# Optimization experiments

Measured on AMD Instinct MI355X. Metric: run time of the kernel, lower is better.

## Reference

```python
import jax, jax.numpy as jnp
import numpy as np

N, E = 50000, 800000
IN_DIM, EDGE_DIM, HID, OUT_DIM, L = 128, 16, 64, 8, 4
MSG_EPS = 1e-7  # GENConv eps added to relu(msg)


def layer_norm(x, g, b, eps=1e-5):
    mu = x.mean(-1, keepdims=True)
    var = ((x - mu) ** 2).mean(-1, keepdims=True)
    return (x - mu) * jax.lax.rsqrt(var + eps) * g + b


def segment_softmax(logits, seg, num_segments):
    # numerically stable softmax over edges grouped by destination node
    m = jax.ops.segment_max(logits, seg, num_segments=num_segments)
    m = jnp.where(jnp.isfinite(m), m, 0.0)
    e = jnp.exp(logits - m[seg])
    s = jax.ops.segment_sum(e, seg, num_segments=num_segments)
    return e / (s[seg] + 1e-16)


def gen_conv(x, src, dst, ea, t, W1, b1, g1, be1, W2, b2):
    # GENConv: message = relu(x_j + e_ij) + eps, softmax-aggregate by dst, add root, MLP [h->2h->h]
    msg = jax.nn.relu(x[src] + ea) + MSG_EPS          # [E, H]
    alpha = segment_softmax(msg * t, dst, x.shape[0]) # [E, H]
    agg = jax.ops.segment_sum(msg * alpha, dst, num_segments=x.shape[0])  # [N, H]
    h = agg + x
    h = jax.nn.relu(layer_norm(h @ W1 + b1, g1, be1))  # [N, 2H]
    return h @ W2 + b2                                 # [N, H]


def setup_inputs() -> dict:
    key = jax.random.key(0)
    ks = jax.random.split(key, 16)
    sc = 0.05
    inp = {
        "x": jax.random.normal(ks[0], (N, IN_DIM), jnp.float32),
        "edge_attr": jax.random.normal(ks[1], (E, EDGE_DIM), jnp.float32),
        "node_W": jax.random.normal(ks[2], (IN_DIM, HID), jnp.float32) * sc,
        "node_b": jnp.zeros((HID,), jnp.float32),
        "edge_W": jax.random.normal(ks[3], (EDGE_DIM, HID), jnp.float32) * sc,
        "edge_b": jnp.zeros((HID,), jnp.float32),
        "conv_t": jnp.ones((L,), jnp.float32),
        "conv_W1": jax.random.normal(ks[4], (L, HID, 2 * HID), jnp.float32) * sc,
        "conv_b1": jnp.zeros((L, 2 * HID), jnp.float32),
        "conv_g1": jnp.ones((L, 2 * HID), jnp.float32),
        "conv_be1": jnp.zeros((L, 2 * HID), jnp.float32),
        "conv_W2": jax.random.normal(ks[5], (L, 2 * HID, HID), jnp.float32) * sc,
        "conv_b2": jnp.zeros((L, HID), jnp.float32),
        "ln_g": jnp.ones((L, HID), jnp.float32),
        "ln_b": jnp.zeros((L, HID), jnp.float32),
        "lin_W": jax.random.normal(ks[6], (HID, OUT_DIM), jnp.float32) * sc,
        "lin_b": jnp.zeros((OUT_DIM,), jnp.float32),
        "edge_index": jax.random.randint(ks[7], (2, E), 0, N, jnp.int64),
    }
    return inp


def reference(x, edge_attr, node_W, node_b, edge_W, edge_b,
              conv_t, conv_W1, conv_b1, conv_g1, conv_be1, conv_W2, conv_b2,
              ln_g, ln_b, lin_W, lin_b, edge_index):
    src, dst = edge_index[0], edge_index[1]  # flow: source_to_target
    h = x @ node_W + node_b
    ea = edge_attr @ edge_W + edge_b
    # first layer: conv only (DeeperGCN applies layers[0].conv directly)
    h = gen_conv(h, src, dst, ea, conv_t[0], conv_W1[0], conv_b1[0],
                 conv_g1[0], conv_be1[0], conv_W2[0], conv_b2[0])
    # res+ blocks: x + conv(dropout(relu(norm(x)))); dropout inactive (eval)
    for i in range(1, L):
        z = jax.nn.relu(layer_norm(h, ln_g[i], ln_b[i]))
        h = h + gen_conv(z, src, dst, ea, conv_t[i], conv_W1[i], conv_b1[i],
                         conv_g1[i], conv_be1[i], conv_W2[i], conv_b2[i])
    h = jax.nn.relu(layer_norm(h, ln_g[0], ln_b[0]))
    return h @ lin_W + lin_b
```

## Files before the change

kernel.cpp:

```cpp
#include <hip/hip_runtime.h>
#include <hip/hip_fp16.h>

#define N_NODES 50000
#define N_EDGES 800000
#define IN_DIM  128
#define EDGE_DIM 16
#define HID     64
#define HID2    128
#define OUT_DIM 8
#define N_LAYERS 4
#define NBUCK   391
#define CCHUNK  4096
#define CBLOCKS 196

typedef _Float16 half8 __attribute__((ext_vector_type(8)));
typedef float floatx4 __attribute__((ext_vector_type(4)));

static __device__ __forceinline__ float bcast(float v, int l) {
    return __uint_as_float(__builtin_amdgcn_readlane(__float_as_uint(v), l));
}

__global__ __launch_bounds__(256, 4) void chist_kernel(
    const int* __restrict__ dsts, int* __restrict__ ccnt)
{
    __shared__ int lh[NBUCK];
    for (int i = threadIdx.x; i < NBUCK; i += 256) lh[i] = 0;
    __syncthreads();
    const int base = blockIdx.x * CCHUNK;
#pragma unroll
    for (int i = 0; i < 16; ++i) {
        const int e = base + i * 256 + threadIdx.x;
        if (e < N_EDGES) atomicAdd(&lh[dsts[e] >> 7], 1);
    }
    __syncthreads();
    for (int i = threadIdx.x; i < NBUCK; i += 256)
        if (lh[i]) atomicAdd(&ccnt[i], lh[i]);
}

__global__ __launch_bounds__(256, 1) void cscan_kernel(
    const int* __restrict__ ccnt, int* __restrict__ coff, int* __restrict__ ccur)
{
    __shared__ int part[512];
    const int t = threadIdx.x;
    part[t]       = (t < NBUCK)       ? ccnt[t]       : 0;
    part[t + 256] = (t + 256 < NBUCK) ? ccnt[t + 256] : 0;
    __syncthreads();
    for (int off = 1; off < 512; off <<= 1) {
        const int v0 = (t >= off) ? part[t - off] : 0;
        const int v1 = (t + 256 >= off) ? part[t + 256 - off] : 0;
        __syncthreads();
        part[t] += v0; part[t + 256] += v1;
        __syncthreads();
    }
    if (t < NBUCK) { const int ex = (t > 0) ? part[t - 1] : 0; coff[t] = ex; ccur[t] = ex; }
    const int i2 = t + 256;
    if (i2 < NBUCK) { coff[i2] = part[i2 - 1]; ccur[i2] = part[i2 - 1]; }
    if (t == 0) coff[NBUCK] = part[NBUCK - 1];
}

__global__ __launch_bounds__(256, 4) void cscatter_kernel(
    const int* __restrict__ srcs, const int* __restrict__ dsts,
    int* __restrict__ ccur, uint2* __restrict__ tmp)
{
    __shared__ int lh[NBUCK], lbase[NBUCK], lrank[NBUCK];
    for (int i = threadIdx.x; i < NBUCK; i += 256) { lh[i] = 0; lrank[i] = 0; }
    __syncthreads();
    const int base = blockIdx.x * CCHUNK;
    int myd[16], mys[16];
#pragma unroll
    for (int i = 0; i < 16; ++i) {
        const int e = base + i * 256 + threadIdx.x;
        if (e < N_EDGES) {
            myd[i] = dsts[e]; mys[i] = srcs[e];
            atomicAdd(&lh[myd[i] >> 7], 1);
        } else myd[i] = -1;
    }
    __syncthreads();
    for (int i = threadIdx.x; i < NBUCK; i += 256) {
        const int c = lh[i];
        lbase[i] = c ? atomicAdd(&ccur[i], c) : 0;
    }
    __syncthreads();
#pragma unroll
    for (int i = 0; i < 16; ++i) {
        if (myd[i] >= 0) {
            const int e = base + i * 256 + threadIdx.x;
            const int b = myd[i] >> 7;
            const int r = atomicAdd(&lrank[b], 1);
            tmp[lbase[b] + r] =
                make_uint2((unsigned)mys[i] | ((unsigned)myd[i] << 16),
                           (unsigned)e);
        }
    }
}

__global__ __launch_bounds__(256, 1) void fsort_kernel(
    const uint2* __restrict__ tmp, const int* __restrict__ coff,
    unsigned* __restrict__ sd2, int* __restrict__ eid)
{
    __shared__ uint2 ebuf[4096];
    __shared__ int lh[128], lsc[128];
    const int b = blockIdx.x;
    const int lo = coff[b];
    const int cnt = coff[b + 1] - lo;
    if (threadIdx.x < 128) lh[threadIdx.x] = 0;
    __syncthreads();
    for (int i = threadIdx.x; i < cnt; i += 256) {
        const uint2 v = tmp[lo + i];
        ebuf[i] = v;
        atomicAdd(&lh[(int)(v.x >> 16) - b * 128], 1);
    }
    __syncthreads();
    if (threadIdx.x < 128) lsc[threadIdx.x] = lh[threadIdx.x];
    __syncthreads();
    for (int off = 1; off < 128; off <<= 1) {
        int v = 0;
        if (threadIdx.x < 128 && threadIdx.x >= off) v = lsc[threadIdx.x - off];
        __syncthreads();
        if (threadIdx.x < 128) lsc[threadIdx.x] += v;
        __syncthreads();
    }
    if (threadIdx.x < 128) lh[threadIdx.x] = lsc[threadIdx.x] - lh[threadIdx.x];
    __syncthreads();
    for (int i = threadIdx.x; i < cnt; i += 256) {
        const uint2 v = ebuf[i];
        const int d = (int)(v.x >> 16) - b * 128;
        const int pos = atomicAdd(&lh[d], 1);
        sd2[lo + pos] = v.x;
        eid[lo + pos] = (int)v.y;
    }
}

__global__ __launch_bounds__(256, 2) void node_proj_kernel(
    const float* __restrict__ x, const float* __restrict__ W,
    const float* __restrict__ b, float* __restrict__ h, __half* __restrict__ zh)
{
    __shared__ float xs[4][IN_DIM];
    const int c = threadIdx.x & 63;
    const int local_n = threadIdx.x >> 6;
    float w[IN_DIM];
#pragma unroll
    for (int k = 0; k < IN_DIM; ++k) w[k] = W[k * HID + c];
    const float bias = b[c];

    for (int base = blockIdx.x * 4; base < N_NODES; base += gridDim.x * 4) {
        __syncthreads();
#pragma unroll
        for (int i = 0; i < 2; ++i) {
            int idx = threadIdx.x + i * 256;
            int nn = idx >> 7, kk = idx & 127;
            xs[nn][kk] = x[(base + nn) * IN_DIM + kk];
        }
        __syncthreads();
        const int n = base + local_n;
        float acc = bias;
#pragma unroll
        for (int k4 = 0; k4 < IN_DIM / 4; ++k4) {
            float4 xv = ((const float4*)xs[local_n])[k4];
            acc = fmaf(xv.x, w[k4 * 4 + 0], acc);
            acc = fmaf(xv.y, w[k4 * 4 + 1], acc);
            acc = fmaf(xv.z, w[k4 * 4 + 2], acc);
            acc = fmaf(xv.w, w[k4 * 4 + 3], acc);
        }
        h[n * HID + c] = acc;
        zh[n * HID + c] = __float2half(acc);
    }
}

__global__ __launch_bounds__(256, 4) void edge_emb_kernel(
    const float* __restrict__ ea, const float* __restrict__ W,
    const float* __restrict__ b, const int* __restrict__ eid,
    __half* __restrict__ eah)
{
    __shared__ __half lds_t[4][16 * HID];
    const int lane = threadIdx.x & 63;
    const int waveid = threadIdx.x >> 6;
    const int wave = (blockIdx.x * 256 + threadIdx.x) >> 6;
    const int nwaves = gridDim.x * 4;
    const int m = lane & 15, q = lane >> 4;
    const int NT = N_EDGES / 16;

    half8 bf[4];
#pragma unroll
    for (int blk = 0; blk < 4; ++blk) {
#pragma unroll
        for (int i = 0; i < 8; ++i) {
            const int k = q * 8 + i;
            bf[blk][i] = (k < EDGE_DIM)
                ? (_Float16)W[k * HID + blk * 16 + m] : (_Float16)0.f;
        }
    }
    float bv[4];
#pragma unroll
    for (int blk = 0; blk < 4; ++blk) bv[blk] = b[blk * 16 + m];

    const int ed = lane >> 3, ch = lane & 7;

    for (int tile = wave; tile < NT; tile += nwaves) {
        const int e0 = tile * 16;
        const int eidx = eid[e0 + m];
        half8 af;
#pragma unroll
        for (int i = 0; i < 8; ++i) af[i] = (_Float16)0.f;
        if (q < 2) {
            const float4* ap =
                (const float4*)(ea + (size_t)eidx * EDGE_DIM + q * 8);
            const float4 lo = ap[0];
            const float4 hi = ap[1];
            af[0] = (_Float16)lo.x; af[1] = (_Float16)lo.y;
            af[2] = (_Float16)lo.z; af[3] = (_Float16)lo.w;
            af[4] = (_Float16)hi.x; af[5] = (_Float16)hi.y;
            af[6] = (_Float16)hi.z; af[7] = (_Float16)hi.w;
        }
        floatx4 c[4];
#pragma unroll
        for (int blk = 0; blk < 4; ++blk) {
            floatx4 cin = {bv[blk], bv[blk], bv[blk], bv[blk]};
            c[blk] = __builtin_amdgcn_mfma_f32_16x16x32_f16(
                af, bf[blk], cin, 0, 0, 0);
        }
#pragma unroll
        for (int blk = 0; blk < 4; ++blk)
#pragma unroll
            for (int r = 0; r < 4; ++r)
                lds_t[waveid][(q * 4 + r) * HID + blk * 16 + m] =
                    __float2half(c[blk][r]);
        const float4 v0 =
            *(const float4*)&lds_t[waveid][ed * HID + ch * 8];
        const float4 v1 =
            *(const float4*)&lds_t[waveid][(8 + ed) * HID + ch * 8];
        ((float4*)(eah + (size_t)(e0 + ed) * HID))[ch] = v0;
        ((float4*)(eah + (size_t)(e0 + 8 + ed) * HID))[ch] = v1;
    }
}

__global__ __launch_bounds__(256, 3) void edge_agg_kernel(
    const __half* __restrict__ zh, const __half* __restrict__ eah,
    const unsigned* __restrict__ sd2,
    const float* __restrict__ conv_t, int layer,
    float* __restrict__ p, float* __restrict__ s)
{
    const int lane = threadIdx.x & 63;
    const int wave = (blockIdx.x * 256 + threadIdx.x) >> 6;
    const int nwaves = gridDim.x * 4;
    const float t2 = conv_t[layer] * 1.4426950408889634f;
    const int NT = N_EDGES / 64;

    const _Float16* zf = (const _Float16*)zh;
    const _Float16* ef = (const _Float16*)eah;

    for (int tile = wave; tile < NT; tile += nwaves) {
        const int e0 = tile * 64;
        const unsigned sdv = sd2[e0 + lane];
        const _Float16* erow = ef + (size_t)e0 * HID + lane;

        _Float16 ez[64];
#pragma unroll
        for (int k = 0; k < 64; ++k) ez[k] = erow[(size_t)k * HID];

        const int sv = (int)(sdv & 0xffffu);
        const int dv = (int)(sdv >> 16);
        const int pv = __shfl_up(dv, 1, 64);
        const unsigned long long bmask = __ballot(dv != pv) & ~1ull;

        _Float16 za[16], zb[16];
#pragma unroll
        for (int k = 0; k < 16; ++k) {
            const int a = __builtin_amdgcn_readlane(sv, k);
            za[k] = zf[(size_t)a * HID + lane];
        }

        float S = 0.f, P = 0.f;
        int cur = __builtin_amdgcn_readlane(dv, 0);
#pragma unroll
        for (int g = 0; g < 4; ++g) {
            if (g < 3) {
#pragma unroll
                for (int k = 0; k < 16; ++k) {
                    const int a = __builtin_amdgcn_readlane(sv, (g + 1) * 16 + k);
                    zb[k] = zf[(size_t)a * HID + lane];
                }
            }
#pragma unroll
            for (int k = 0; k < 16; ++k) {
                const int j = g * 16 + k;
                if (bmask & (1ull << j)) {
                    unsafeAtomicAdd(&s[(size_t)cur * HID + lane], S);
                    unsafeAtomicAdd(&p[(size_t)cur * HID + lane], P);
                    S = 0.f; P = 0.f;
                    cur = __builtin_amdgcn_readlane(dv, j);
                }
                _Float16 mh = za[k] + ez[j];
                mh = mh > (_Float16)0.f ? mh : (_Float16)0.f;
                const float mm = (float)mh + 1e-7f;
                const float xx = __builtin_amdgcn_exp2f(mm * t2);
                S += xx;
                P = fmaf(mm, xx, P);
            }
            if (g < 3) {
#pragma unroll
                for (int k = 0; k < 16; ++k) za[k] = zb[k];
            }
        }
        unsafeAtomicAdd(&s[(size_t)cur * HID + lane], S);
        unsafeAtomicAdd(&p[(size_t)cur * HID + lane], P);
    }
}

__global__ __launch_bounds__(256, 3) void node_mm1_kernel(
    float* __restrict__ p, float* __restrict__ s,
    const __half* __restrict__ zh,
    const float* __restrict__ W1, const float* __restrict__ b1,
    const float* __restrict__ g1, const float* __restrict__ be1,
    __half* __restrict__ vh)
{
    const int lane = threadIdx.x & 63;
    const int wave = (blockIdx.x * 256 + threadIdx.x) >> 6;
    const int nwaves = gridDim.x * 4;

    float wa[HID], wb[HID];
#pragma unroll
    for (int k = 0; k < HID; ++k) {
        wa[k] = W1[k * HID2 + lane];
        wb[k] = W1[k * HID2 + 64 + lane];
    }
    const float ba = b1[lane],  bb = b1[64 + lane];
    const float ga = g1[lane],  gb = g1[64 + lane];
    const float ca = be1[lane], cb = be1[64 + lane];

    for (int n = wave; n < N_NODES; n += nwaves) {
        const int idx = n * HID + lane;
        const float pv = p[idx];
        const float sv = s[idx];
        const float zv = __half2float(zh[idx]);
        p[idx] = 0.f;
        s[idx] = 0.f;
        const float hv = pv / (sv + 1e-16f) + zv;

        float a0 = 0.f, a1 = 0.f, c0 = 0.f, c1 = 0.f;
#pragma unroll
        for (int k = 0; k < 32; ++k) {
            const float x0 = bcast(hv, k);
            const float x1 = bcast(hv, k + 32);
            a0 = fmaf(x0, wa[k], a0);
            c0 = fmaf(x0, wb[k], c0);
            a1 = fmaf(x1, wa[k + 32], a1);
            c1 = fmaf(x1, wb[k + 32], c1);
        }
        const float ua = (a0 + a1) + ba;
        const float ub = (c0 + c1) + bb;

        float sum = ua + ub;
#pragma unroll
        for (int o = 1; o < 64; o <<= 1) sum += __shfl_xor(sum, o, 64);
        const float mu = sum * (1.f / 128.f);
        const float da = ua - mu, db = ub - mu;
        float q = fmaf(da, da, db * db);
#pragma unroll
        for (int o = 1; o < 64; o <<= 1) q += __shfl_xor(q, o, 64);
        const float rstd = rsqrtf(q * (1.f / 128.f) + 1e-5f);
        const float ya = da * rstd * ga + ca;
        const float yb = db * rstd * gb + cb;
        vh[(size_t)n * HID2 + lane]      = __float2half(ya > 0.f ? ya : 0.f);
        vh[(size_t)n * HID2 + 64 + lane] = __float2half(yb > 0.f ? yb : 0.f);
    }
}

__global__ __launch_bounds__(256, 3) void node_mm2_kernel(
    const __half* __restrict__ vh,
    const float* __restrict__ W2, const float* __restrict__ b2,
    const float* __restrict__ lng, const float* __restrict__ lnb,
    float* __restrict__ h, __half* __restrict__ zh, int residual)
{
    const int lane = threadIdx.x & 63;
    const int wave = (blockIdx.x * 256 + threadIdx.x) >> 6;
    const int nwaves = gridDim.x * 4;

    float wa[HID2 / 2], wb[HID2 / 2];
#pragma unroll
    for (int k = 0; k < HID2 / 2; ++k) {
        wa[k] = W2[k * HID + lane];
        wb[k] = W2[(k + 64) * HID + lane];
    }
    const float bias = b2[lane];
    const float g = lng[lane];
    const float be = lnb[lane];

    for (int n = wave; n < N_NODES; n += nwaves) {
        const float f0 = __half2float(vh[(size_t)n * HID2 + lane]);
        const float f1 = __half2float(vh[(size_t)n * HID2 + 64 + lane]);

        float a0 = 0.f, a1 = 0.f, c0 = 0.f, c1 = 0.f;
#pragma unroll
        for (int k = 0; k < 32; ++k) {
            const float x0 = bcast(f0, k);
            const float x1 = bcast(f0, k + 32);
            const float x2 = bcast(f1, k);
            const float x3 = bcast(f1, k + 32);
            a0 = fmaf(x0, wa[k], a0);
            a1 = fmaf(x1, wa[k + 32], a1);
            c0 = fmaf(x2, wb[k], c0);
            c1 = fmaf(x3, wb[k + 32], c1);
        }
        const float acc = (a0 + a1) + (c0 + c1) + bias;

        const int idx = n * HID + lane;
        const float hn = residual ? (h[idx] + acc) : acc;
        h[idx] = hn;

        float sum = hn;
#pragma unroll
        for (int o = 1; o < 64; o <<= 1) sum += __shfl_xor(sum, o, 64);
        const float mu = sum * (1.f / 64.f);
        const float d = hn - mu;
        float q = d * d;
#pragma unroll
        for (int o = 1; o < 64; o <<= 1) q += __shfl_xor(q, o, 64);
        const float var = q * (1.f / 64.f);
        const float y = d * rsqrtf(var + 1e-5f) * g + be;
        zh[idx] = __float2half(y > 0.f ? y : 0.f);
    }
}

__global__ __launch_bounds__(256, 4) void final_kernel(
    const __half* __restrict__ zh, const float* __restrict__ Wl,
    const float* __restrict__ bl, float* __restrict__ out)
{
    __shared__ float wl[HID * OUT_DIM];
    for (int i = threadIdx.x; i < HID * OUT_DIM; i += 256) wl[i] = Wl[i];
    __syncthreads();
    const int total = N_NODES * OUT_DIM;
    for (int idx = blockIdx.x * 256 + threadIdx.x; idx < total;
         idx += gridDim.x * 256) {
        const int n = idx >> 3, o = idx & 7;
        const __half2* zp = (const __half2*)(zh + (size_t)n * HID);
        float acc = bl[o];
#pragma unroll
        for (int k2 = 0; k2 < HID / 2; ++k2) {
            const float2 f = __half22float2(zp[k2]);
            acc = fmaf(f.x, wl[(k2 * 2 + 0) * OUT_DIM + o], acc);
            acc = fmaf(f.y, wl[(k2 * 2 + 1) * OUT_DIM + o], acc);
        }
        out[idx] = acc;
    }
}

extern "C" void kernel_launch(void* const* d_in, const int* in_sizes, int n_in,
                              void* d_out, int out_size, void* d_ws, size_t ws_size,
                              hipStream_t stream)
{
    const float* x         = (const float*)d_in[0];
    const float* edge_attr = (const float*)d_in[1];
    const float* node_W    = (const float*)d_in[2];
    const float* node_b    = (const float*)d_in[3];
    const float* edge_W    = (const float*)d_in[4];
    const float* edge_b    = (const float*)d_in[5];
    const float* conv_t    = (const float*)d_in[6];
    const float* conv_W1   = (const float*)d_in[7];
    const float* conv_b1   = (const float*)d_in[8];
    const float* conv_g1   = (const float*)d_in[9];
    const float* conv_be1  = (const float*)d_in[10];
    const float* conv_W2   = (const float*)d_in[11];
    const float* conv_b2   = (const float*)d_in[12];
    const float* ln_g      = (const float*)d_in[13];
    const float* ln_b      = (const float*)d_in[14];
    const float* lin_W     = (const float*)d_in[15];
    const float* lin_b     = (const float*)d_in[16];
    const int*   edge_index= (const int*)d_in[17];
    const int*   srcs = edge_index;
    const int*   dsts = edge_index + N_EDGES;
    float* out = (float*)d_out;

    float* h   = (float*)d_ws;
    float* p   = h   + N_NODES * HID;
    float* s   = p   + N_NODES * HID;
    __half* vh  = (__half*)(s + N_NODES * HID);
    __half* zh  = vh + (size_t)N_NODES * HID2;
    __half* eah = zh + (size_t)N_NODES * HID;
    uint2* tmp  = (uint2*)(eah + (size_t)N_EDGES * HID);
    unsigned* sd2 = (unsigned*)(tmp + N_EDGES);
    int* eid    = (int*)(sd2 + N_EDGES);
    int* ccnt   = eid + N_EDGES;
    int* coff   = ccnt + NBUCK;
    int* ccur   = coff + NBUCK + 1;

    hipMemsetAsync(ccnt, 0, (size_t)NBUCK * sizeof(int), stream);
    chist_kernel<<<CBLOCKS, 256, 0, stream>>>(dsts, ccnt);
    cscan_kernel<<<1, 256, 0, stream>>>(ccnt, coff, ccur);
    cscatter_kernel<<<CBLOCKS, 256, 0, stream>>>(srcs, dsts, ccur, tmp);
    fsort_kernel<<<NBUCK, 256, 0, stream>>>(tmp, coff, sd2, eid);

    node_proj_kernel<<<2048, 256, 0, stream>>>(x, node_W, node_b, h, zh);
    edge_emb_kernel<<<3125, 256, 0, stream>>>(edge_attr, edge_W, edge_b, eid, eah);

    hipMemsetAsync(p, 0, (size_t)2 * N_NODES * HID * sizeof(float), stream);

    for (int layer = 0; layer < N_LAYERS; ++layer) {
        edge_agg_kernel<<<3125, 256, 0, stream>>>(zh, eah, sd2,
                                                  conv_t, layer, p, s);
        node_mm1_kernel<<<2048, 256, 0, stream>>>(
            p, s, zh,
            conv_W1 + (size_t)layer * HID * HID2, conv_b1 + layer * HID2,
            conv_g1 + layer * HID2, conv_be1 + layer * HID2, vh);
        const float* gz = (layer < N_LAYERS - 1) ? (ln_g + (layer + 1) * HID) : ln_g;
        const float* bz = (layer < N_LAYERS - 1) ? (ln_b + (layer + 1) * HID) : ln_b;
        node_mm2_kernel<<<2048, 256, 0, stream>>>(
            vh, conv_W2 + (size_t)layer * HID2 * HID, conv_b2 + layer * HID,
            gz, bz, h, zh, layer > 0 ? 1 : 0);
    }
    final_kernel<<<1024, 256, 0, stream>>>(zh, lin_W, lin_b, out);
}
```

Before: 673.9 us.

## Interleave softmax accumulators and store interior segments directly instead of atomics

The separate p and s accumulators are merged into one interleaved float2 array, so each node's numerator and denominator share a cache line and node_mm1 reads and clears both with a single vector access. In edge_agg, a destination segment that lies entirely inside a 64-edge tile (neither the first nor the last segment of the tile) is written with a plain store rather than two atomics, since edges are sorted by destination and no other tile touches that node. The edge_emb launch grid also grows from 3125 to 12500 blocks. The plain store relies on interior segments being exclusively owned by one tile, which holds only because the edges are sorted by destination.

```diff
diff --git a/kernel.cpp b/kernel.cpp
--- a/kernel.cpp
+++ b/kernel.cpp
@@ -238,7 +238,7 @@
     const __half* __restrict__ zh, const __half* __restrict__ eah,
     const unsigned* __restrict__ sd2,
     const float* __restrict__ conv_t, int layer,
-    float* __restrict__ p, float* __restrict__ s)
+    float2* __restrict__ ps)
 {
     const int lane = threadIdx.x & 63;
     const int wave = (blockIdx.x * 256 + threadIdx.x) >> 6;
@@ -272,6 +272,7 @@
 
         float S = 0.f, P = 0.f;
         int cur = __builtin_amdgcn_readlane(dv, 0);
+        bool first = true;
 #pragma unroll
         for (int g = 0; g < 4; ++g) {
             if (g < 3) {
@@ -285,8 +286,14 @@
             for (int k = 0; k < 16; ++k) {
                 const int j = g * 16 + k;
                 if (bmask & (1ull << j)) {
-                    unsafeAtomicAdd(&s[(size_t)cur * HID + lane], S);
-                    unsafeAtomicAdd(&p[(size_t)cur * HID + lane], P);
+                    float2* addr = &ps[(size_t)cur * HID + lane];
+                    if (first) {
+                        unsafeAtomicAdd(&addr->x, P);
+                        unsafeAtomicAdd(&addr->y, S);
+                        first = false;
+                    } else {
+                        *addr = make_float2(P, S);
+                    }
                     S = 0.f; P = 0.f;
                     cur = __builtin_amdgcn_readlane(dv, j);
                 }
@@ -302,13 +309,16 @@
                 for (int k = 0; k < 16; ++k) za[k] = zb[k];
             }
         }
-        unsafeAtomicAdd(&s[(size_t)cur * HID + lane], S);
-        unsafeAtomicAdd(&p[(size_t)cur * HID + lane], P);
+        {
+            float2* addr = &ps[(size_t)cur * HID + lane];
+            unsafeAtomicAdd(&addr->x, P);
+            unsafeAtomicAdd(&addr->y, S);
+        }
     }
 }
 
 __global__ __launch_bounds__(256, 3) void node_mm1_kernel(
-    float* __restrict__ p, float* __restrict__ s,
+    float2* __restrict__ ps,
     const __half* __restrict__ zh,
     const float* __restrict__ W1, const float* __restrict__ b1,
     const float* __restrict__ g1, const float* __restrict__ be1,
@@ -330,12 +340,10 @@
 
     for (int n = wave; n < N_NODES; n += nwaves) {
         const int idx = n * HID + lane;
-        const float pv = p[idx];
-        const float sv = s[idx];
+        const float2 pv2 = ps[idx];
         const float zv = __half2float(zh[idx]);
-        p[idx] = 0.f;
-        s[idx] = 0.f;
-        const float hv = pv / (sv + 1e-16f) + zv;
+        ps[idx] = make_float2(0.f, 0.f);
+        const float hv = pv2.x / (pv2.y + 1e-16f) + zv;
 
         float a0 = 0.f, a1 = 0.f, c0 = 0.f, c1 = 0.f;
 #pragma unroll
@@ -471,10 +479,9 @@
     const int*   dsts = edge_index + N_EDGES;
     float* out = (float*)d_out;
 
-    float* h   = (float*)d_ws;
-    float* p   = h   + N_NODES * HID;
-    float* s   = p   + N_NODES * HID;
-    __half* vh  = (__half*)(s + N_NODES * HID);
+    float* h    = (float*)d_ws;
+    float2* ps  = (float2*)(h + N_NODES * HID);
+    __half* vh  = (__half*)(ps + N_NODES * HID);
     __half* zh  = vh + (size_t)N_NODES * HID2;
     __half* eah = zh + (size_t)N_NODES * HID;
     uint2* tmp  = (uint2*)(eah + (size_t)N_EDGES * HID);
@@ -491,15 +498,15 @@
     fsort_kernel<<<NBUCK, 256, 0, stream>>>(tmp, coff, sd2, eid);
 
     node_proj_kernel<<<2048, 256, 0, stream>>>(x, node_W, node_b, h, zh);
-    edge_emb_kernel<<<3125, 256, 0, stream>>>(edge_attr, edge_W, edge_b, eid, eah);
-
-    hipMemsetAsync(p, 0, (size_t)2 * N_NODES * HID * sizeof(float), stream);
+    edge_emb_kernel<<<12500, 256, 0, stream>>>(edge_attr, edge_W, edge_b, eid, eah);
+
+    hipMemsetAsync(ps, 0, (size_t)N_NODES * HID * sizeof(float2), stream);
 
     for (int layer = 0; layer < N_LAYERS; ++layer) {
         edge_agg_kernel<<<3125, 256, 0, stream>>>(zh, eah, sd2,
-                                                  conv_t, layer, p, s);
+                                                  conv_t, layer, ps);
         node_mm1_kernel<<<2048, 256, 0, stream>>>(
-            p, s, zh,
+            ps, zh,
             conv_W1 + (size_t)layer * HID * HID2, conv_b1 + layer * HID2,
             conv_g1 + layer * HID2, conv_be1 + layer * HID2, vh);
         const float* gz = (layer < N_LAYERS - 1) ? (ln_g + (layer + 1) * HID) : ln_g;
```

Result: slower. 712.5 us (+5.7%).
